# Optimization experiments

Hardware: AMD Instinct MI355X
Metric: run time of the kernel (lower is better)

Reference implementation:

```python
import jax, jax.numpy as jnp
import numpy as np

D_MODEL = 512
N_HEADS = 8
D_HEAD = D_MODEL // N_HEADS
SCALE = 1.0 / np.sqrt(D_MODEL).astype(np.float32)  # source divides by sqrt(d_model), not sqrt(d_head)


def setup_inputs() -> dict:
    key = jax.random.key(0)
    ks = jax.random.split(key, 9)
    B, S = 4, 2048
    std = 1.0 / np.sqrt(D_MODEL).astype(np.float32)
    x = jax.random.normal(ks[0], (B, S, D_MODEL), dtype=jnp.float32)
    Wq = jax.random.normal(ks[1], (D_MODEL, D_MODEL), dtype=jnp.float32) * std
    bq = jnp.zeros((D_MODEL,), jnp.float32)
    Wk = jax.random.normal(ks[2], (D_MODEL, D_MODEL), dtype=jnp.float32) * std
    bk = jnp.zeros((D_MODEL,), jnp.float32)
    Wv = jax.random.normal(ks[3], (D_MODEL, D_MODEL), dtype=jnp.float32) * std
    bv = jnp.zeros((D_MODEL,), jnp.float32)
    Wo = jax.random.normal(ks[4], (D_MODEL, D_MODEL), dtype=jnp.float32) * std
    bo = jnp.zeros((D_MODEL,), jnp.float32)
    return {"x": x, "Wq": Wq, "bq": bq, "Wk": Wk, "bk": bk,
            "Wv": Wv, "bv": bv, "Wo": Wo, "bo": bo}


def reference(x, Wq, bq, Wk, bk, Wv, bv, Wo, bo):
    B, S, _ = x.shape
    # projections -> [B, H, S, Dh]
    def split_heads(t):
        return t.reshape(B, S, N_HEADS, D_HEAD).transpose(0, 2, 1, 3)
    q = split_heads(x @ Wq + bq)
    k = split_heads(x @ Wk + bk)
    v = split_heads(x @ Wv + bv)
    # scores: [B, H, S, S], scaled by 1/sqrt(d_model) as in source
    scores = jnp.einsum('bhqd,bhkd->bhqk', q, k) * SCALE
    weights = jax.nn.softmax(scores, axis=-1)
    # dropout is identity at inference time
    att = jnp.einsum('bhqk,bhkd->bhqd', weights, v)
    att = att.transpose(0, 2, 1, 3).reshape(B, S, D_MODEL)
    return att @ Wo + bo
```

## Files before the change

kernel.cpp:

```cpp
#include <hip/hip_runtime.h>
#include <math.h>

#define BATCH   4
#define S_LEN   2048
#define DMODEL  512
#define NHEADS  8
#define DHEAD   64
#define M_TOT   8192
#define ATT_SCALE 0.04419417382415922f

using short8  = __attribute__((ext_vector_type(8))) short;
using floatx4 = __attribute__((ext_vector_type(4))) float;

__device__ __forceinline__ ushort f2bf(float f) {
    union { float f; unsigned u; } x; x.f = f;
    unsigned u = x.u + 0x7FFFu + ((x.u >> 16) & 1u);
    return (ushort)(u >> 16);
}
__device__ __forceinline__ unsigned pk2(float a, float b) {
    return (unsigned)f2bf(a) | ((unsigned)f2bf(b) << 16);
}
__device__ __forceinline__ unsigned pkr2(float a, float b) {
    unsigned ua = __float_as_uint(a) + 0x8000u;
    unsigned ub = __float_as_uint(b) + 0x8000u;
    return __builtin_amdgcn_perm(ub, ua, 0x07060302u);
}

__global__ __launch_bounds__(256) void conv_x(const float* __restrict__ x,
                                              ushort* __restrict__ xb)
{
    const int i = (blockIdx.x * 256 + threadIdx.x) * 4;
    float4 f = *(const float4*)(x + i);
    uint2 o; o.x = pk2(f.x, f.y); o.y = pk2(f.z, f.w);
    *(uint2*)(xb + i) = o;
}

__global__ __launch_bounds__(256) void transp_w(
    const float* __restrict__ Wq, const float* __restrict__ Wk,
    const float* __restrict__ Wv, const float* __restrict__ Wo,
    ushort* __restrict__ WT)
{
    const int p  = blockIdx.z;
    const float* W = (p == 0) ? Wq : (p == 1) ? Wk : (p == 2) ? Wv : Wo;
    const int n  = blockIdx.y * 256 + threadIdx.x;
    const int k0 = blockIdx.x * 16;
    unsigned u[8];
    #pragma unroll
    for (int j = 0; j < 8; ++j) {
        float a = W[(k0 + 2 * j)     * DMODEL + n];
        float b = W[(k0 + 2 * j + 1) * DMODEL + n];
        u[j] = pk2(a, b);
    }
    ushort* dst = WT + ((size_t)p * DMODEL + n) * DMODEL + k0;
    *(uint4*)dst       = *(uint4*)&u[0];
    *(uint4*)(dst + 8) = *(uint4*)&u[4];
}

__global__ __launch_bounds__(256, 4) void qkv_gemm(
    const ushort* __restrict__ xb, const ushort* __restrict__ WT,
    const float* __restrict__ bq, const float* __restrict__ bk, const float* __restrict__ bv,
    ushort* __restrict__ q, ushort* __restrict__ k, ushort* __restrict__ vT)
{
    __shared__ ushort SMEM[128 * 136];
    ushort (*A)[40] = (ushort(*)[40])SMEM;
    ushort (*B)[40] = (ushort(*)[40])(SMEM + 128 * 40);
    ushort (*CT)[136] = (ushort(*)[136])SMEM;

    const int tid = threadIdx.x;
    const int wv  = tid >> 6, lane = tid & 63, l16 = lane & 15, quad = lane >> 4;
    const int m0  = blockIdx.x * 128;
    const int ng0 = blockIdx.y * 128;
    const int p   = ng0 >> 9;
    const int n0  = ng0 & 511;
    const ushort* Wp  = WT + (size_t)p * DMODEL * DMODEL + (size_t)n0 * DMODEL;
    const float* bias = (p == 0) ? bq : (p == 1) ? bk : bv;

    const int wm = (wv & 1) * 64, wn = (wv >> 1) * 64;
    floatx4 acc[4][4] = {};

    const int ar = tid >> 1, ac = (tid & 1) * 16;

    for (int k0 = 0; k0 < DMODEL; k0 += 32) {
        uint4 a0 = *(const uint4*)(xb + (size_t)(m0 + ar) * DMODEL + k0 + ac);
        uint4 a1 = *(const uint4*)(xb + (size_t)(m0 + ar) * DMODEL + k0 + ac + 8);
        uint4 b0 = *(const uint4*)(Wp + (size_t)ar * DMODEL + k0 + ac);
        uint4 b1 = *(const uint4*)(Wp + (size_t)ar * DMODEL + k0 + ac + 8);
        *(uint4*)&A[ar][ac] = a0; *(uint4*)&A[ar][ac + 8] = a1;
        *(uint4*)&B[ar][ac] = b0; *(uint4*)&B[ar][ac + 8] = b1;
        __syncthreads();

        short8 af[4], bf[4];
        #pragma unroll
        for (int i = 0; i < 4; ++i) af[i] = *(const short8*)&A[wm + i * 16 + l16][quad * 8];
        #pragma unroll
        for (int c = 0; c < 4; ++c) bf[c] = *(const short8*)&B[wn + c * 16 + l16][quad * 8];
        #pragma unroll
        for (int i = 0; i < 4; ++i)
            #pragma unroll
            for (int c = 0; c < 4; ++c)
                acc[i][c] = __builtin_amdgcn_mfma_f32_16x16x32_bf16(af[i], bf[c], acc[i][c], 0, 0, 0);
        __syncthreads();
    }

    if (p < 2) {
        #pragma unroll
        for (int c = 0; c < 4; ++c) {
            const int n = n0 + wn + c * 16 + l16;
            const float bb = bias[n];
            const int h = n >> 6, dh = n & 63;
            #pragma unroll
            for (int i = 0; i < 4; ++i)
                #pragma unroll
                for (int r = 0; r < 4; ++r) {
                    const int m = m0 + wm + i * 16 + quad * 4 + r;
                    const int b = m >> 11, s = m & 2047;
                    const ushort val = f2bf(acc[i][c][r] + bb);
                    if (p == 0) q[((size_t)(b * NHEADS + h) * S_LEN + s) * DHEAD + dh] = val;
                    else        k[((size_t)(b * NHEADS + h) * S_LEN + s) * DHEAD + dh] = val;
                }
        }
    } else {
        #pragma unroll
        for (int c = 0; c < 4; ++c) {
            const int n = wn + c * 16 + l16;
            const float bb = bias[n0 + n];
            #pragma unroll
            for (int i = 0; i < 4; ++i) {
                uint2 o;
                o.x = pk2(acc[i][c][0] + bb, acc[i][c][1] + bb);
                o.y = pk2(acc[i][c][2] + bb, acc[i][c][3] + bb);
                *(uint2*)&CT[n][wm + i * 16 + quad * 4] = o;
            }
        }
        __syncthreads();
        const int n  = tid >> 1, mh = (tid & 1) * 64;
        const int gn = n0 + n;
        const int h  = gn >> 6, dh = gn & 63;
        const int b  = m0 >> 11, sb = (m0 & 2047) + mh;
        ushort* dst = vT + ((size_t)(b * NHEADS + h) * DHEAD + dh) * S_LEN + sb;
        #pragma unroll
        for (int j = 0; j < 8; ++j)
            *(uint4*)(dst + j * 8) = *(const uint4*)&CT[n][mh + j * 8];
    }
}

__global__ __launch_bounds__(256, 2) void attn(
    const ushort* __restrict__ Q, const ushort* __restrict__ K,
    const ushort* __restrict__ vT, ushort* __restrict__ att)
{
    __shared__ ushort Klds[64][72];
    __shared__ ushort Vt[64][72];
    __shared__ ushort Plds[128][72];

    const int tid = threadIdx.x;
    const int wv  = tid >> 6, lane = tid & 63, l16 = lane & 15, quad = lane >> 4;
    const int q0  = blockIdx.x * 128;
    const int bh  = blockIdx.y;
    const ushort* Qh = Q  + (size_t)bh * S_LEN * DHEAD;
    const ushort* Kh = K  + (size_t)bh * S_LEN * DHEAD;
    const ushort* Vh = vT + (size_t)bh * DHEAD * S_LEN;

    short8 qf[2][2];
    #pragma unroll
    for (int ni = 0; ni < 2; ++ni) {
        const ushort* qrow = Qh + (size_t)(q0 + wv * 32 + ni * 16 + l16) * DHEAD;
        qf[0][ni] = *(const short8*)(qrow + quad * 8);
        qf[1][ni] = *(const short8*)(qrow + 32 + quad * 8);
    }

    floatx4 oacc[4][2] = {};
    float lsum[2] = {0.f, 0.f};

    const int srow = tid >> 2, sc0 = (tid & 3) * 16;
    uint4 ka, kb, va, vb;
    {
        const ushort* Ks = Kh + (size_t)srow * DHEAD + sc0;
        const ushort* Vs = Vh + (size_t)srow * S_LEN + sc0;
        ka = *(const uint4*)Ks; kb = *(const uint4*)(Ks + 8);
        va = *(const uint4*)Vs; vb = *(const uint4*)(Vs + 8);
    }

    for (int kt = 0; kt < S_LEN / 64; ++kt) {
        *(uint4*)&Klds[srow][sc0] = ka; *(uint4*)&Klds[srow][sc0 + 8] = kb;
        *(uint4*)&Vt[srow][sc0]   = va; *(uint4*)&Vt[srow][sc0 + 8]   = vb;
        __syncthreads();

        if (kt + 1 < S_LEN / 64) {
            const ushort* Ks = Kh + (size_t)((kt + 1) * 64 + srow) * DHEAD + sc0;
            const ushort* Vs = Vh + (size_t)srow * S_LEN + (kt + 1) * 64 + sc0;
            ka = *(const uint4*)Ks; kb = *(const uint4*)(Ks + 8);
            va = *(const uint4*)Vs; vb = *(const uint4*)(Vs + 8);
        }

        floatx4 sc[4][2] = {};
        #pragma unroll
        for (int s = 0; s < 2; ++s)
            #pragma unroll
            for (int mi = 0; mi < 4; ++mi) {
                short8 kf = *(const short8*)&Klds[mi * 16 + l16][s * 32 + quad * 8];
                #pragma unroll
                for (int ni = 0; ni < 2; ++ni)
                    sc[mi][ni] = __builtin_amdgcn_mfma_f32_16x16x32_bf16(kf, qf[s][ni], sc[mi][ni], 0, 0, 0);
            }

        #pragma unroll
        for (int mi = 0; mi < 4; ++mi)
            #pragma unroll
            for (int ni = 0; ni < 2; ++ni) {
                const float p0 = __expf(sc[mi][ni][0] * ATT_SCALE);
                const float p1 = __expf(sc[mi][ni][1] * ATT_SCALE);
                const float p2 = __expf(sc[mi][ni][2] * ATT_SCALE);
                const float p3 = __expf(sc[mi][ni][3] * ATT_SCALE);
                lsum[ni] += (p0 + p1) + (p2 + p3);
                uint2 o; o.x = pkr2(p0, p1); o.y = pkr2(p2, p3);
                *(uint2*)&Plds[wv * 32 + ni * 16 + l16][mi * 16 + quad * 4] = o;
            }

        #pragma unroll
        for (int s = 0; s < 2; ++s) {
            short8 pf[2];
            #pragma unroll
            for (int ni = 0; ni < 2; ++ni)
                pf[ni] = *(const short8*)&Plds[wv * 32 + ni * 16 + l16][s * 32 + quad * 8];
            #pragma unroll
            for (int mi = 0; mi < 4; ++mi) {
                short8 vf = *(const short8*)&Vt[mi * 16 + l16][s * 32 + quad * 8];
                #pragma unroll
                for (int ni = 0; ni < 2; ++ni)
                    oacc[mi][ni] = __builtin_amdgcn_mfma_f32_16x16x32_bf16(vf, pf[ni], oacc[mi][ni], 0, 0, 0);
            }
        }
        __syncthreads();
    }

    #pragma unroll
    for (int ni = 0; ni < 2; ++ni) {
        float t = lsum[ni];
        t += __shfl_xor(t, 16, 64);
        t += __shfl_xor(t, 32, 64);
        lsum[ni] = 1.f / t;
    }

    const int b = bh >> 3, h = bh & 7;
    #pragma unroll
    for (int ni = 0; ni < 2; ++ni) {
        const int qi = q0 + wv * 32 + ni * 16 + l16;
        ushort* dst = att + ((size_t)(b * S_LEN + qi)) * DMODEL + h * DHEAD;
        #pragma unroll
        for (int mi = 0; mi < 4; ++mi) {
            uint2 o;
            o.x = pk2(oacc[mi][ni][0] * lsum[ni], oacc[mi][ni][1] * lsum[ni]);
            o.y = pk2(oacc[mi][ni][2] * lsum[ni], oacc[mi][ni][3] * lsum[ni]);
            *(uint2*)(dst + mi * 16 + quad * 4) = o;
        }
    }
}

__global__ __launch_bounds__(256, 4) void out_gemm(
    const ushort* __restrict__ att, const ushort* __restrict__ WoT,
    const float* __restrict__ bo, float* __restrict__ out)
{
    __shared__ ushort A[128][40];
    __shared__ ushort B[128][40];

    const int tid = threadIdx.x;
    const int wv  = tid >> 6, lane = tid & 63, l16 = lane & 15, quad = lane >> 4;
    const int m0 = blockIdx.x * 128;
    const int n0 = blockIdx.y * 128;

    const int wm = (wv & 1) * 64, wn = (wv >> 1) * 64;
    floatx4 acc[4][4] = {};
    const int ar = tid >> 1, ac = (tid & 1) * 16;

    for (int k0 = 0; k0 < DMODEL; k0 += 32) {
        uint4 a0 = *(const uint4*)(att + (size_t)(m0 + ar) * DMODEL + k0 + ac);
        uint4 a1 = *(const uint4*)(att + (size_t)(m0 + ar) * DMODEL + k0 + ac + 8);
        uint4 b0 = *(const uint4*)(WoT + (size_t)(n0 + ar) * DMODEL + k0 + ac);
        uint4 b1 = *(const uint4*)(WoT + (size_t)(n0 + ar) * DMODEL + k0 + ac + 8);
        *(uint4*)&A[ar][ac] = a0; *(uint4*)&A[ar][ac + 8] = a1;
        *(uint4*)&B[ar][ac] = b0; *(uint4*)&B[ar][ac + 8] = b1;
        __syncthreads();

        short8 af[4], bf[4];
        #pragma unroll
        for (int i = 0; i < 4; ++i) af[i] = *(const short8*)&A[wm + i * 16 + l16][quad * 8];
        #pragma unroll
        for (int c = 0; c < 4; ++c) bf[c] = *(const short8*)&B[wn + c * 16 + l16][quad * 8];
        #pragma unroll
        for (int i = 0; i < 4; ++i)
            #pragma unroll
            for (int c = 0; c < 4; ++c)
                acc[i][c] = __builtin_amdgcn_mfma_f32_16x16x32_bf16(af[i], bf[c], acc[i][c], 0, 0, 0);
        __syncthreads();
    }

    #pragma unroll
    for (int c = 0; c < 4; ++c) {
        const int n = n0 + wn + c * 16 + l16;
        const float bb = bo[n];
        #pragma unroll
        for (int i = 0; i < 4; ++i)
            #pragma unroll
            for (int r = 0; r < 4; ++r) {
                const int m = m0 + wm + i * 16 + quad * 4 + r;
                out[(size_t)m * DMODEL + n] = acc[i][c][r] + bb;
            }
    }
}

extern "C" void kernel_launch(void* const* d_in, const int* in_sizes, int n_in,
                              void* d_out, int out_size, void* d_ws, size_t ws_size,
                              hipStream_t stream)
{
    const float* x  = (const float*)d_in[0];
    const float* Wq = (const float*)d_in[1];
    const float* bq = (const float*)d_in[2];
    const float* Wk = (const float*)d_in[3];
    const float* bk = (const float*)d_in[4];
    const float* Wv = (const float*)d_in[5];
    const float* bv = (const float*)d_in[6];
    const float* Wo = (const float*)d_in[7];
    const float* bo = (const float*)d_in[8];
    float* out = (float*)d_out;

    ushort* ws = (ushort*)d_ws;
    const size_t SZ = (size_t)M_TOT * DMODEL;
    ushort* xb  = ws;
    ushort* att = ws;
    ushort* WT  = ws + SZ;
    ushort* q   = WT + 4 * (size_t)DMODEL * DMODEL;
    ushort* k   = q + SZ;
    ushort* vT  = k + SZ;

    conv_x  <<<M_TOT * DMODEL / (256 * 4), 256, 0, stream>>>(x, xb);
    transp_w<<<dim3(DMODEL / 16, DMODEL / 256, 4), 256, 0, stream>>>(Wq, Wk, Wv, Wo, WT);

    qkv_gemm<<<dim3(M_TOT / 128, 3 * DMODEL / 128), 256, 0, stream>>>(
        xb, WT, bq, bk, bv, q, k, vT);

    attn<<<dim3(S_LEN / 128, BATCH * NHEADS), 256, 0, stream>>>(q, k, vT, att);

    out_gemm<<<dim3(M_TOT / 128, DMODEL / 128), 256, 0, stream>>>(
        att, WT + 3 * (size_t)DMODEL * DMODEL, bo, out);
}
```

Baseline: 179.3 us.

## Split attention over key range with combine pass, fold scale into Q

Attention work is split across two key-range chunks via a third grid dimension, writing fp32 partial outputs and row sums that a new combine kernel merges. The grid doubles from 512 blocks and launch bounds rise to 4 waves per SIMD, both aimed at higher occupancy. The softmax scale and log2(e) are folded into Q at projection time so the inner loop can use raw exp2. The x conversion and weight transpose kernels are merged into one launch. The split path adds fp32 partial-output traffic and an extra kernel, and only runs if the workspace is large enough.

```diff
diff --git a/kernel.cpp b/kernel.cpp
--- a/kernel.cpp
+++ b/kernel.cpp
@@ -8,6 +8,7 @@
 #define DHEAD   64
 #define M_TOT   8192
 #define ATT_SCALE 0.04419417382415922f
+#define QSCALE (ATT_SCALE * 1.44269504088896f)
 
 using short8  = __attribute__((ext_vector_type(8))) short;
 using floatx4 = __attribute__((ext_vector_type(4))) float;
@@ -26,34 +27,36 @@
     return __builtin_amdgcn_perm(ub, ua, 0x07060302u);
 }
 
-__global__ __launch_bounds__(256) void conv_x(const float* __restrict__ x,
-                                              ushort* __restrict__ xb)
-{
-    const int i = (blockIdx.x * 256 + threadIdx.x) * 4;
-    float4 f = *(const float4*)(x + i);
-    uint2 o; o.x = pk2(f.x, f.y); o.y = pk2(f.z, f.w);
-    *(uint2*)(xb + i) = o;
-}
-
-__global__ __launch_bounds__(256) void transp_w(
+__global__ __launch_bounds__(256) void prep(
+    const float* __restrict__ x,
     const float* __restrict__ Wq, const float* __restrict__ Wk,
     const float* __restrict__ Wv, const float* __restrict__ Wo,
-    ushort* __restrict__ WT)
-{
-    const int p  = blockIdx.z;
-    const float* W = (p == 0) ? Wq : (p == 1) ? Wk : (p == 2) ? Wv : Wo;
-    const int n  = blockIdx.y * 256 + threadIdx.x;
-    const int k0 = blockIdx.x * 16;
-    unsigned u[8];
-    #pragma unroll
-    for (int j = 0; j < 8; ++j) {
-        float a = W[(k0 + 2 * j)     * DMODEL + n];
-        float b = W[(k0 + 2 * j + 1) * DMODEL + n];
-        u[j] = pk2(a, b);
-    }
-    ushort* dst = WT + ((size_t)p * DMODEL + n) * DMODEL + k0;
-    *(uint4*)dst       = *(uint4*)&u[0];
-    *(uint4*)(dst + 8) = *(uint4*)&u[4];
+    ushort* __restrict__ xb, ushort* __restrict__ WT)
+{
+    const int bid = blockIdx.x;
+    if (bid < 4096) {
+        const int i = (bid * 256 + threadIdx.x) * 4;
+        float4 f = *(const float4*)(x + i);
+        uint2 o; o.x = pk2(f.x, f.y); o.y = pk2(f.z, f.w);
+        *(uint2*)(xb + i) = o;
+    } else {
+        const int rb = bid - 4096;
+        const int p  = rb >> 6;
+        const int rem = rb & 63;
+        const int n  = (rem >> 5) * 256 + threadIdx.x;
+        const int k0 = (rem & 31) * 16;
+        const float* W = (p == 0) ? Wq : (p == 1) ? Wk : (p == 2) ? Wv : Wo;
+        unsigned u[8];
+        #pragma unroll
+        for (int j = 0; j < 8; ++j) {
+            float a = W[(k0 + 2 * j)     * DMODEL + n];
+            float b = W[(k0 + 2 * j + 1) * DMODEL + n];
+            u[j] = pk2(a, b);
+        }
+        ushort* dst = WT + ((size_t)p * DMODEL + n) * DMODEL + k0;
+        *(uint4*)dst       = *(uint4*)&u[0];
+        *(uint4*)(dst + 8) = *(uint4*)&u[4];
+    }
 }
 
 __global__ __launch_bounds__(256, 4) void qkv_gemm(
@@ -74,10 +77,10 @@
     const int n0  = ng0 & 511;
     const ushort* Wp  = WT + (size_t)p * DMODEL * DMODEL + (size_t)n0 * DMODEL;
     const float* bias = (p == 0) ? bq : (p == 1) ? bk : bv;
+    const float scl   = (p == 0) ? QSCALE : 1.0f;
 
     const int wm = (wv & 1) * 64, wn = (wv >> 1) * 64;
     floatx4 acc[4][4] = {};
-
     const int ar = tid >> 1, ac = (tid & 1) * 16;
 
     for (int k0 = 0; k0 < DMODEL; k0 += 32) {
@@ -114,7 +117,7 @@
                 for (int r = 0; r < 4; ++r) {
                     const int m = m0 + wm + i * 16 + quad * 4 + r;
                     const int b = m >> 11, s = m & 2047;
-                    const ushort val = f2bf(acc[i][c][r] + bb);
+                    const ushort val = f2bf((acc[i][c][r] + bb) * scl);
                     if (p == 0) q[((size_t)(b * NHEADS + h) * S_LEN + s) * DHEAD + dh] = val;
                     else        k[((size_t)(b * NHEADS + h) * S_LEN + s) * DHEAD + dh] = val;
                 }
@@ -144,9 +147,11 @@
     }
 }
 
-__global__ __launch_bounds__(256, 2) void attn(
+__global__ __launch_bounds__(256, 4) void attn(
     const ushort* __restrict__ Q, const ushort* __restrict__ K,
-    const ushort* __restrict__ vT, ushort* __restrict__ att)
+    const ushort* __restrict__ vT, ushort* __restrict__ att,
+    float* __restrict__ Opart, float* __restrict__ Lpart,
+    const int KT, const int direct)
 {
     __shared__ ushort Klds[64][72];
     __shared__ ushort Vt[64][72];
@@ -156,6 +161,8 @@
     const int wv  = tid >> 6, lane = tid & 63, l16 = lane & 15, quad = lane >> 4;
     const int q0  = blockIdx.x * 128;
     const int bh  = blockIdx.y;
+    const int ck  = blockIdx.z;
+    const int kbase = ck * KT;
     const ushort* Qh = Q  + (size_t)bh * S_LEN * DHEAD;
     const ushort* Kh = K  + (size_t)bh * S_LEN * DHEAD;
     const ushort* Vh = vT + (size_t)bh * DHEAD * S_LEN;
@@ -174,20 +181,20 @@
     const int srow = tid >> 2, sc0 = (tid & 3) * 16;
     uint4 ka, kb, va, vb;
     {
-        const ushort* Ks = Kh + (size_t)srow * DHEAD + sc0;
-        const ushort* Vs = Vh + (size_t)srow * S_LEN + sc0;
+        const ushort* Ks = Kh + (size_t)(kbase * 64 + srow) * DHEAD + sc0;
+        const ushort* Vs = Vh + (size_t)srow * S_LEN + kbase * 64 + sc0;
         ka = *(const uint4*)Ks; kb = *(const uint4*)(Ks + 8);
         va = *(const uint4*)Vs; vb = *(const uint4*)(Vs + 8);
     }
 
-    for (int kt = 0; kt < S_LEN / 64; ++kt) {
+    for (int kt = 0; kt < KT; ++kt) {
         *(uint4*)&Klds[srow][sc0] = ka; *(uint4*)&Klds[srow][sc0 + 8] = kb;
         *(uint4*)&Vt[srow][sc0]   = va; *(uint4*)&Vt[srow][sc0 + 8]   = vb;
         __syncthreads();
 
-        if (kt + 1 < S_LEN / 64) {
-            const ushort* Ks = Kh + (size_t)((kt + 1) * 64 + srow) * DHEAD + sc0;
-            const ushort* Vs = Vh + (size_t)srow * S_LEN + (kt + 1) * 64 + sc0;
+        if (kt + 1 < KT) {
+            const ushort* Ks = Kh + (size_t)((kbase + kt + 1) * 64 + srow) * DHEAD + sc0;
+            const ushort* Vs = Vh + (size_t)srow * S_LEN + (kbase + kt + 1) * 64 + sc0;
             ka = *(const uint4*)Ks; kb = *(const uint4*)(Ks + 8);
             va = *(const uint4*)Vs; vb = *(const uint4*)(Vs + 8);
         }
@@ -207,10 +214,10 @@
         for (int mi = 0; mi < 4; ++mi)
             #pragma unroll
             for (int ni = 0; ni < 2; ++ni) {
-                const float p0 = __expf(sc[mi][ni][0] * ATT_SCALE);
-                const float p1 = __expf(sc[mi][ni][1] * ATT_SCALE);
-                const float p2 = __expf(sc[mi][ni][2] * ATT_SCALE);
-                const float p3 = __expf(sc[mi][ni][3] * ATT_SCALE);
+                const float p0 = __builtin_amdgcn_exp2f(sc[mi][ni][0]);
+                const float p1 = __builtin_amdgcn_exp2f(sc[mi][ni][1]);
+                const float p2 = __builtin_amdgcn_exp2f(sc[mi][ni][2]);
+                const float p3 = __builtin_amdgcn_exp2f(sc[mi][ni][3]);
                 lsum[ni] += (p0 + p1) + (p2 + p3);
                 uint2 o; o.x = pkr2(p0, p1); o.y = pkr2(p2, p3);
                 *(uint2*)&Plds[wv * 32 + ni * 16 + l16][mi * 16 + quad * 4] = o;
@@ -233,27 +240,66 @@
         __syncthreads();
     }
 
+    float tot[2];
     #pragma unroll
     for (int ni = 0; ni < 2; ++ni) {
         float t = lsum[ni];
         t += __shfl_xor(t, 16, 64);
         t += __shfl_xor(t, 32, 64);
-        lsum[ni] = 1.f / t;
-    }
-
-    const int b = bh >> 3, h = bh & 7;
-    #pragma unroll
-    for (int ni = 0; ni < 2; ++ni) {
-        const int qi = q0 + wv * 32 + ni * 16 + l16;
-        ushort* dst = att + ((size_t)(b * S_LEN + qi)) * DMODEL + h * DHEAD;
-        #pragma unroll
-        for (int mi = 0; mi < 4; ++mi) {
-            uint2 o;
-            o.x = pk2(oacc[mi][ni][0] * lsum[ni], oacc[mi][ni][1] * lsum[ni]);
-            o.y = pk2(oacc[mi][ni][2] * lsum[ni], oacc[mi][ni][3] * lsum[ni]);
-            *(uint2*)(dst + mi * 16 + quad * 4) = o;
-        }
-    }
+        tot[ni] = t;
+    }
+
+    if (direct) {
+        const int b = bh >> 3, h = bh & 7;
+        #pragma unroll
+        for (int ni = 0; ni < 2; ++ni) {
+            const float inv = 1.f / tot[ni];
+            const int qi = q0 + wv * 32 + ni * 16 + l16;
+            ushort* dst = att + ((size_t)(b * S_LEN + qi)) * DMODEL + h * DHEAD;
+            #pragma unroll
+            for (int mi = 0; mi < 4; ++mi) {
+                uint2 o;
+                o.x = pk2(oacc[mi][ni][0] * inv, oacc[mi][ni][1] * inv);
+                o.y = pk2(oacc[mi][ni][2] * inv, oacc[mi][ni][3] * inv);
+                *(uint2*)(dst + mi * 16 + quad * 4) = o;
+            }
+        }
+    } else {
+        #pragma unroll
+        for (int ni = 0; ni < 2; ++ni) {
+            const int qi = q0 + wv * 32 + ni * 16 + l16;
+            const size_t row = (size_t)(ck * 32 + bh) * S_LEN + qi;
+            if (quad == 0) Lpart[row] = tot[ni];
+            #pragma unroll
+            for (int mi = 0; mi < 4; ++mi) {
+                float4 o = { oacc[mi][ni][0], oacc[mi][ni][1],
+                             oacc[mi][ni][2], oacc[mi][ni][3] };
+                *(float4*)&Opart[row * DHEAD + mi * 16 + quad * 4] = o;
+            }
+        }
+    }
+}
+
+__global__ __launch_bounds__(256) void combine(
+    const float* __restrict__ Opart, const float* __restrict__ Lpart,
+    ushort* __restrict__ att)
+{
+    const int idx = blockIdx.x * 256 + threadIdx.x;
+    const int row = idx >> 3;
+    const int dho = (idx & 7) * 8;
+    const int bh = row >> 11, qq = row & 2047;
+    const float* o0 = Opart + (size_t)row * DHEAD + dho;
+    const float* o1 = Opart + (size_t)(65536 + row) * DHEAD + dho;
+    float4 a0 = *(const float4*)o0,       a1 = *(const float4*)(o0 + 4);
+    float4 b0 = *(const float4*)o1,       b1 = *(const float4*)(o1 + 4);
+    const float inv = 1.f / (Lpart[row] + Lpart[65536 + row]);
+    uint4 u;
+    u.x = pk2((a0.x + b0.x) * inv, (a0.y + b0.y) * inv);
+    u.y = pk2((a0.z + b0.z) * inv, (a0.w + b0.w) * inv);
+    u.z = pk2((a1.x + b1.x) * inv, (a1.y + b1.y) * inv);
+    u.w = pk2((a1.z + b1.z) * inv, (a1.w + b1.w) * inv);
+    ushort* dst = att + ((size_t)((bh >> 3) * S_LEN + qq)) * DMODEL + (bh & 7) * DHEAD + dho;
+    *(uint4*)dst = u;
 }
 
 __global__ __launch_bounds__(256, 4) void out_gemm(
@@ -331,14 +377,23 @@
     ushort* q   = WT + 4 * (size_t)DMODEL * DMODEL;
     ushort* k   = q + SZ;
     ushort* vT  = k + SZ;
-
-    conv_x  <<<M_TOT * DMODEL / (256 * 4), 256, 0, stream>>>(x, xb);
-    transp_w<<<dim3(DMODEL / 16, DMODEL / 256, 4), 256, 0, stream>>>(Wq, Wk, Wv, Wo, WT);
+    float*  Opart = (float*)(vT + SZ);
+    float*  Lpart = Opart + 2 * (size_t)32 * S_LEN * DHEAD;
+
+    const size_t base_need  = (size_t)(vT + SZ - ws) * 2;
+    const size_t split_need = base_need + 2 * ((size_t)32 * S_LEN * DHEAD + 32 * S_LEN) * 4;
+    const int SPLIT = (ws_size >= split_need) ? 2 : 1;
+
+    prep<<<4096 + 256, 256, 0, stream>>>(x, Wq, Wk, Wv, Wo, xb, WT);
 
     qkv_gemm<<<dim3(M_TOT / 128, 3 * DMODEL / 128), 256, 0, stream>>>(
         xb, WT, bq, bk, bv, q, k, vT);
 
-    attn<<<dim3(S_LEN / 128, BATCH * NHEADS), 256, 0, stream>>>(q, k, vT, att);
+    attn<<<dim3(S_LEN / 128, BATCH * NHEADS, SPLIT), 256, 0, stream>>>(
+        q, k, vT, att, Opart, Lpart, S_LEN / 64 / SPLIT, SPLIT == 1 ? 1 : 0);
+
+    if (SPLIT == 2)
+        combine<<<(32 * S_LEN * DHEAD / 8) / 256, 256, 0, stream>>>(Opart, Lpart, att);
 
     out_gemm<<<dim3(M_TOT / 128, DMODEL / 128), 256, 0, stream>>>(
         att, WT + 3 * (size_t)DMODEL * DMODEL, bo, out);
```

New measurement: 181.8 us. About the same (+1.4%).
